# Kernel tuning notes

Measured on AMD Instinct MI355X. Metric: run time of the kernel, lower is better.

The kernel has to match this reference:

```python
import jax, jax.numpy as jnp
import numpy as np

B, LQ, LK, C = 16, 1024, 1024, 512
WH = int(LQ ** 0.5)  # 32


def setup_inputs() -> dict:
    key = jax.random.key(0)
    ks = jax.random.split(key, 6)
    s1 = 1.0 / np.sqrt(LK)
    return {
        "query": jax.random.normal(ks[0], (B, LQ, C), jnp.float32),
        "key": jax.random.normal(ks[1], (B, LK, C), jnp.float32),
        "value": jax.random.normal(ks[2], (B, LK, C), jnp.float32),
        # nn.Linear weights, stored [out_features, in_features] like torch
        "w1": jax.random.normal(ks[3], (LK, LK), jnp.float32) * s1,
        "w2": jax.random.normal(ks[4], (LK, LK), jnp.float32) * s1,
        "w3": jax.random.normal(ks[5], (1, LK), jnp.float32) * s1,
    }


def reference(query, key, value, w1, w2, w3):
    # cosine-similarity matrix (computed under no_grad in the original)
    q = query / 100.0
    k = key / 100.0
    qn = jnp.sqrt(jnp.sum(q * q, axis=-1))[:, :, None]   # [B, LQ, 1]
    kn = jnp.sqrt(jnp.sum(k * k, axis=-1))[:, None, :]   # [B, 1, LK]
    outer = qn * kn                                       # rank-1 outer product [B, LQ, LK]
    upper = jnp.einsum('bqc,bkc->bqk', q, k)              # [B, LQ, LK]
    similar_rev = jax.lax.stop_gradient(upper / (outer + 1e-6))

    # 3-layer MLP gating over the LK axis -> scalar weight per query row
    h = jax.nn.gelu(jnp.einsum('bqk,ok->bqo', similar_rev, w1), approximate=False)
    h = jax.nn.gelu(jnp.einsum('bqk,ok->bqo', h, w2), approximate=False)
    w = jnp.einsum('bqk,ok->bqo', h, w3)[..., 0]          # [B, LQ]

    # weight^T @ similar_rev / wh, then tanh -> per-key scalar gate [B, LK, 1]
    weight = jnp.einsum('bq,bqk->bk', w, similar_rev) / WH
    weight = jnp.tanh(weight)[:, :, None]

    # value modulation + residual
    return value * weight + value
```

## Files before the change

kernel.cpp:

```cpp
#include <hip/hip_runtime.h>
#include <hip/hip_bf16.h>

#define B_  16
#define LQ_ 1024
#define LK_ 1024
#define C_  512

typedef __attribute__((ext_vector_type(4))) float f32x4;
typedef __attribute__((ext_vector_type(8))) short bf16x8;

__device__ __forceinline__ float bf2f(ushort u) {
  union { unsigned int i; float f; } v; v.i = ((unsigned int)u) << 16; return v.f;
}
__device__ __forceinline__ ushort f2bf(float f) {
  union { float f; unsigned int i; } v; v.f = f;
  unsigned int r = v.i + 0x7fffu + ((v.i >> 16) & 1u);
  return (ushort)(r >> 16);
}
__device__ __forceinline__ float gelu_exact(float x) {
  return 0.5f * x * (1.0f + erff(x * 0.70710678118654752f));
}

__global__ __launch_bounds__(256) void prep_qk(const float* __restrict__ x,
                                               ushort* __restrict__ xb,
                                               float* __restrict__ norms) {
  int wid = blockIdx.x * 4 + (threadIdx.x >> 6);
  int lane = threadIdx.x & 63;
  const float* xr = x + (long)wid * C_;
  ushort* xo = xb + (long)wid * C_;
  float ss = 0.f;
#pragma unroll
  for (int i0 = 0; i0 < 2; ++i0) {
    int i = lane * 4 + i0 * 256;
    float4 v = *(const float4*)(xr + i);
    ss += v.x * v.x + v.y * v.y + v.z * v.z + v.w * v.w;
    ushort4 o;
    o.x = f2bf(v.x); o.y = f2bf(v.y); o.z = f2bf(v.z); o.w = f2bf(v.w);
    *(ushort4*)(xo + i) = o;
  }
#pragma unroll
  for (int off = 32; off > 0; off >>= 1) ss += __shfl_xor(ss, off);
  if (lane == 0) norms[wid] = sqrtf(ss);
}

__global__ __launch_bounds__(256) void conv_bf16(const float* __restrict__ x,
                                                 ushort* __restrict__ o, int n4) {
  int i = blockIdx.x * 256 + threadIdx.x;
  if (i < n4) {
    float4 v = *(const float4*)(x + (long)i * 4);
    ushort4 u;
    u.x = f2bf(v.x); u.y = f2bf(v.y); u.z = f2bf(v.z); u.w = f2bf(v.w);
    *(ushort4*)(o + (long)i * 4) = u;
  }
}

#define BK 32
#define LDT 40

template <int EPI>
__global__ __launch_bounds__(256, 2) void gemm_nt(
    const ushort* __restrict__ A, const ushort* __restrict__ Bm,
    ushort* __restrict__ Cc, int K, long sA, long sB, long sC,
    const float* __restrict__ qn, const float* __restrict__ kn) {
  int b = blockIdx.z;
  A += (long)b * sA;
  Bm += (long)b * sB;
  Cc += (long)b * sC;
  const int bm = blockIdx.y * 128, bn = blockIdx.x * 128;

  __shared__ ushort At[128][LDT];
  __shared__ ushort Bt[128][LDT];

  int tid = threadIdx.x;
  int lane = tid & 63, w = tid >> 6;
  int wr = w >> 1, wc = w & 1;
  int l16 = lane & 15, lhi = lane >> 4;

  f32x4 acc[4][4] = {};

  for (int k0 = 0; k0 < K; k0 += BK) {
    __syncthreads();
#pragma unroll
    for (int i = 0; i < 2; ++i) {
      int chunk = tid + 256 * i;
      int row = chunk >> 2, cb = chunk & 3;
      *(bf16x8*)&At[row][cb * 8] =
          *(const bf16x8*)(A + (long)(bm + row) * K + k0 + cb * 8);
      *(bf16x8*)&Bt[row][cb * 8] =
          *(const bf16x8*)(Bm + (long)(bn + row) * K + k0 + cb * 8);
    }
    __syncthreads();

    bf16x8 af[4], bfr[4];
#pragma unroll
    for (int m = 0; m < 4; ++m)
      af[m] = *(const bf16x8*)&At[wr * 64 + m * 16 + l16][lhi * 8];
#pragma unroll
    for (int n = 0; n < 4; ++n)
      bfr[n] = *(const bf16x8*)&Bt[wc * 64 + n * 16 + l16][lhi * 8];
#pragma unroll
    for (int m = 0; m < 4; ++m)
#pragma unroll
      for (int n = 0; n < 4; ++n)
        acc[m][n] = __builtin_amdgcn_mfma_f32_16x16x32_bf16(af[m], bfr[n],
                                                            acc[m][n], 0, 0, 0);
  }

#pragma unroll
  for (int m = 0; m < 4; ++m) {
    int row0 = bm + wr * 64 + m * 16 + lhi * 4;
#pragma unroll
    for (int n = 0; n < 4; ++n) {
      int col = bn + wc * 64 + n * 16 + l16;
#pragma unroll
      for (int r = 0; r < 4; ++r) {
        float v = acc[m][n][r];
        int grow = row0 + r;
        if (EPI == 0) {
          v = v / (qn[grow] * kn[col] + 1e-2f);
        } else {
          v = gelu_exact(v);
        }
        Cc[(long)grow * 1024 + col] = f2bf(v);
      }
    }
  }
}

__global__ __launch_bounds__(256) void wdot(const ushort* __restrict__ h2,
                                            const float* __restrict__ w3,
                                            float* __restrict__ wv) {
  int row = blockIdx.x * 4 + (threadIdx.x >> 6);
  int lane = threadIdx.x & 63;
  const ushort* hr = h2 + (long)row * LK_;
  float acc = 0.f;
#pragma unroll
  for (int i = 0; i < 2; ++i) {
    int idx = (lane + 64 * i) * 8;
    bf16x8 v = *(const bf16x8*)(hr + idx);
#pragma unroll
    for (int j = 0; j < 8; ++j) acc += bf2f((ushort)v[j]) * w3[idx + j];
  }
#pragma unroll
  for (int off = 32; off > 0; off >>= 1) acc += __shfl_xor(acc, off);
  if (lane == 0) wv[row] = acc;
}

__global__ __launch_bounds__(256) void gate_partial(const ushort* __restrict__ S,
                                                    const float* __restrict__ wv,
                                                    float* __restrict__ wraw) {
  int b = blockIdx.z;
  int k = blockIdx.x * 256 + threadIdx.x;
  int q0 = blockIdx.y * 128;
  const ushort* Sb = S + (long)b * LQ_ * LK_;
  const float* wb = wv + b * LQ_;
  float acc = 0.f;
#pragma unroll 4
  for (int q = q0; q < q0 + 128; ++q) acc += wb[q] * bf2f(Sb[(long)q * LK_ + k]);
  atomicAdd(&wraw[b * LK_ + k], acc);
}

__global__ __launch_bounds__(256) void finalize(const float* __restrict__ value,
                                                const float* __restrict__ wraw,
                                                float* __restrict__ out) {
  long i = (long)blockIdx.x * 256 + threadIdx.x;
  long e = i * 4;
  int row = (int)(e >> 9);
  float g = 1.f + tanhf(wraw[row] * (1.f / 32.f));
  float4 v = ((const float4*)value)[i];
  v.x *= g; v.y *= g; v.z *= g; v.w *= g;
  ((float4*)out)[i] = v;
}

extern "C" void kernel_launch(void* const* d_in, const int* in_sizes, int n_in,
                              void* d_out, int out_size, void* d_ws,
                              size_t ws_size, hipStream_t stream) {
  const float* query = (const float*)d_in[0];
  const float* key   = (const float*)d_in[1];
  const float* value = (const float*)d_in[2];
  const float* w1    = (const float*)d_in[3];
  const float* w2    = (const float*)d_in[4];
  const float* w3    = (const float*)d_in[5];
  float* out = (float*)d_out;

  const size_t QB_BYTES = (size_t)B_ * LQ_ * C_ * 2;
  const size_t S_BYTES  = (size_t)B_ * LQ_ * LK_ * 2;
  const size_t W_BYTES  = (size_t)LK_ * LK_ * 2;
  const size_t OFF_QB = 0;
  const size_t OFF_KB = OFF_QB + QB_BYTES;
  const size_t OFF_H2 = 0;
  const size_t OFF_S  = OFF_KB + QB_BYTES;
  const size_t OFF_H1 = OFF_S + S_BYTES;
  const size_t OFF_W1 = OFF_H1 + S_BYTES;
  const size_t OFF_W2 = OFF_W1 + W_BYTES;
  const size_t OFF_QN = OFF_W2 + W_BYTES;
  const size_t OFF_KN = OFF_QN + (size_t)B_ * LQ_ * 4;
  const size_t OFF_WV = OFF_KN + (size_t)B_ * LK_ * 4;
  const size_t OFF_WR = OFF_WV + (size_t)B_ * LQ_ * 4;
  const size_t TOTAL  = OFF_WR + (size_t)B_ * LK_ * 4;
  if (ws_size < TOTAL) return;

  char* ws = (char*)d_ws;
  ushort* Qb  = (ushort*)(ws + OFF_QB);
  ushort* Kb  = (ushort*)(ws + OFF_KB);
  ushort* S   = (ushort*)(ws + OFF_S);
  ushort* h1  = (ushort*)(ws + OFF_H1);
  ushort* h2  = (ushort*)(ws + OFF_H2);
  ushort* W1b = (ushort*)(ws + OFF_W1);
  ushort* W2b = (ushort*)(ws + OFF_W2);
  float* qn   = (float*)(ws + OFF_QN);
  float* kn   = (float*)(ws + OFF_KN);
  float* wv   = (float*)(ws + OFF_WV);
  float* wraw = (float*)(ws + OFF_WR);

  prep_qk<<<dim3(B_ * LQ_ / 4), 256, 0, stream>>>(query, Qb, qn);
  prep_qk<<<dim3(B_ * LK_ / 4), 256, 0, stream>>>(key, Kb, kn);
  conv_bf16<<<dim3(LK_ * LK_ / 4 / 256), 256, 0, stream>>>(w1, W1b, LK_ * LK_ / 4);
  conv_bf16<<<dim3(LK_ * LK_ / 4 / 256), 256, 0, stream>>>(w2, W2b, LK_ * LK_ / 4);
  hipMemsetAsync(wraw, 0, (size_t)B_ * LK_ * 4, stream);

  gemm_nt<0><<<dim3(8, 8, B_), 256, 0, stream>>>(
      Qb, Kb, S, C_, (long)LQ_ * C_, (long)LK_ * C_, (long)LQ_ * LK_, qn, kn);

  gemm_nt<1><<<dim3(8, 8, B_), 256, 0, stream>>>(
      S, W1b, h1, LK_, (long)LQ_ * LK_, 0L, (long)LQ_ * LK_, nullptr, nullptr);

  gemm_nt<1><<<dim3(8, 8, B_), 256, 0, stream>>>(
      h1, W2b, h2, LK_, (long)LQ_ * LK_, 0L, (long)LQ_ * LK_, nullptr, nullptr);

  wdot<<<dim3(B_ * LQ_ / 4), 256, 0, stream>>>(h2, w3, wv);

  gate_partial<<<dim3(LK_ / 256, LQ_ / 128, B_), 256, 0, stream>>>(S, wv, wraw);

  finalize<<<dim3((size_t)B_ * LK_ * C_ / 4 / 256), 256, 0, stream>>>(value, wraw, out);
}
```

Baseline: 202.9 us.

## Rewrite GEMMs as 256x256 double-buffered direct-to-LDS tiles and fuse w3 dot

Replaces the 128x128 single-buffered GEMM with a 256x256 tile, 512-thread kernel. It uses global_load_lds direct-to-LDS loads, XOR-swizzled LDS, double buffering with prefetch interleaved with MFMA phases, and s_setprio. It remaps the grid so blocks of the same batch land on the same XCD for L2 reuse. The third GEMM's epilogue now applies GELU and the w3 dot product with atomics into wv, which removes the h2 write and the separate wdot kernel. The risks are 256 blocks giving only one wave of occupancy on 256 CUs, atomic summation order, and LDS usage of 128KB per block.

```diff
diff --git a/kernel.cpp b/kernel.cpp
--- a/kernel.cpp
+++ b/kernel.cpp
@@ -19,6 +19,12 @@
 }
 __device__ __forceinline__ float gelu_exact(float x) {
   return 0.5f * x * (1.0f + erff(x * 0.70710678118654752f));
+}
+
+__device__ __forceinline__ void gload_lds16(const ushort* g, ushort* l) {
+  __builtin_amdgcn_global_load_lds(
+      (const __attribute__((address_space(1))) void*)g,
+      (__attribute__((address_space(3))) void*)l, 16, 0, 0);
 }
 
 __global__ __launch_bounds__(256) void prep_qk(const float* __restrict__ x,
@@ -54,96 +60,164 @@
   }
 }
 
-#define BK 32
-#define LDT 40
-
 template <int EPI>
-__global__ __launch_bounds__(256, 2) void gemm_nt(
+__global__ __launch_bounds__(512, 2) void gemm256(
     const ushort* __restrict__ A, const ushort* __restrict__ Bm,
     ushort* __restrict__ Cc, int K, long sA, long sB, long sC,
-    const float* __restrict__ qn, const float* __restrict__ kn) {
-  int b = blockIdx.z;
+    const float* __restrict__ qn, const float* __restrict__ kn,
+    const float* __restrict__ w3v, float* __restrict__ wv) {
+  int per = (int)(gridDim.x >> 3);
+  int orig = blockIdx.x;
+  int id = (orig & 7) * per + (orig >> 3);
+  int b = id >> 4;
+  int rt = id & 15;
+  const int bm = (rt >> 2) * 256, bn = (rt & 3) * 256;
+
   A += (long)b * sA;
   Bm += (long)b * sB;
-  Cc += (long)b * sC;
-  const int bm = blockIdx.y * 128, bn = blockIdx.x * 128;
-
-  __shared__ ushort At[128][LDT];
-  __shared__ ushort Bt[128][LDT];
-
-  int tid = threadIdx.x;
-  int lane = tid & 63, w = tid >> 6;
-  int wr = w >> 1, wc = w & 1;
-  int l16 = lane & 15, lhi = lane >> 4;
-
-  f32x4 acc[4][4] = {};
-
-  for (int k0 = 0; k0 < K; k0 += BK) {
-    __syncthreads();
-#pragma unroll
-    for (int i = 0; i < 2; ++i) {
-      int chunk = tid + 256 * i;
-      int row = chunk >> 2, cb = chunk & 3;
-      *(bf16x8*)&At[row][cb * 8] =
-          *(const bf16x8*)(A + (long)(bm + row) * K + k0 + cb * 8);
-      *(bf16x8*)&Bt[row][cb * 8] =
-          *(const bf16x8*)(Bm + (long)(bn + row) * K + k0 + cb * 8);
+
+  __shared__ ushort At[2][256][64];
+  __shared__ ushort Bt[2][256][64];
+  const int bufStride = 256 * 64;
+
+  const int tid = threadIdx.x;
+  const int lane = tid & 63, w = tid >> 6;
+  const int wr = w >> 2, wc = w & 3;
+  const int l16 = lane & 15, lhi = lane >> 4;
+
+  f32x4 acc[8][4] = {};
+
+  const ushort* gA[4];
+  const ushort* gB[4];
+  ushort* lA[4];
+  ushort* lB[4];
+#pragma unroll
+  for (int i = 0; i < 4; ++i) {
+    int c = i * 512 + tid;
+    int row = c >> 3;
+    int cb = (c & 7) ^ (row & 7);
+    gA[i] = A + (long)(bm + row) * K + cb * 8;
+    gB[i] = Bm + (long)(bn + row) * K + cb * 8;
+    int wch = i * 512 + (tid & ~63);
+    lA[i] = &At[0][0][0] + (size_t)wch * 8;
+    lB[i] = &Bt[0][0][0] + (size_t)wch * 8;
+  }
+
+#pragma unroll
+  for (int i = 0; i < 4; ++i) {
+    gload_lds16(gA[i], lA[i]);
+    gload_lds16(gB[i], lB[i]);
+  }
+  asm volatile("s_waitcnt vmcnt(0)" ::: "memory");
+  __builtin_amdgcn_s_barrier();
+
+  const int nt = K / 64;
+  int cur = 0;
+  for (int t = 0; t < nt; ++t) {
+    const int koff = (t + 1) * 64;
+    const bool pf = (t + 1 < nt);
+    const ushort* Acur = &At[cur][0][0];
+    const ushort* Bcur = &Bt[cur][0][0];
+    const size_t nxo = (size_t)(cur ^ 1) * bufStride;
+
+    bf16x8 bfr[4][2];
+
+#pragma unroll
+    for (int p = 0; p < 4; ++p) {
+      bf16x8 af[2][2];
+#pragma unroll
+      for (int e = 0; e < 2; ++e)
+#pragma unroll
+        for (int kk = 0; kk < 2; ++kk) {
+          int r = wr * 128 + (p * 2 + e) * 16 + l16;
+          af[e][kk] = *(const bf16x8*)(Acur + r * 64 +
+                                       (((kk * 4 + lhi) ^ (r & 7)) * 8));
+        }
+      if (p == 0) {
+#pragma unroll
+        for (int n = 0; n < 4; ++n)
+#pragma unroll
+          for (int kk = 0; kk < 2; ++kk) {
+            int r = wc * 64 + n * 16 + l16;
+            bfr[n][kk] = *(const bf16x8*)(Bcur + r * 64 +
+                                          (((kk * 4 + lhi) ^ (r & 7)) * 8));
+          }
+      }
+      if (pf) {
+        if (p == 0) {
+          gload_lds16(gA[0] + koff, lA[0] + nxo);
+          gload_lds16(gA[1] + koff, lA[1] + nxo);
+          gload_lds16(gB[0] + koff, lB[0] + nxo);
+        } else if (p == 1) {
+          gload_lds16(gA[2] + koff, lA[2] + nxo);
+          gload_lds16(gA[3] + koff, lA[3] + nxo);
+          gload_lds16(gB[1] + koff, lB[1] + nxo);
+        } else if (p == 2) {
+          gload_lds16(gB[2] + koff, lB[2] + nxo);
+          gload_lds16(gB[3] + koff, lB[3] + nxo);
+        }
+      }
+      __builtin_amdgcn_s_barrier();
+      __builtin_amdgcn_s_setprio(1);
+#pragma unroll
+      for (int e = 0; e < 2; ++e)
+#pragma unroll
+        for (int n = 0; n < 4; ++n)
+#pragma unroll
+          for (int kk = 0; kk < 2; ++kk)
+            acc[p * 2 + e][n] = __builtin_amdgcn_mfma_f32_16x16x32_bf16(
+                af[e][kk], bfr[n][kk], acc[p * 2 + e][n], 0, 0, 0);
+      __builtin_amdgcn_s_setprio(0);
+      if (p == 3) asm volatile("s_waitcnt vmcnt(0)" ::: "memory");
+      __builtin_amdgcn_s_barrier();
     }
-    __syncthreads();
-
-    bf16x8 af[4], bfr[4];
-#pragma unroll
-    for (int m = 0; m < 4; ++m)
-      af[m] = *(const bf16x8*)&At[wr * 64 + m * 16 + l16][lhi * 8];
-#pragma unroll
-    for (int n = 0; n < 4; ++n)
-      bfr[n] = *(const bf16x8*)&Bt[wc * 64 + n * 16 + l16][lhi * 8];
-#pragma unroll
-    for (int m = 0; m < 4; ++m)
-#pragma unroll
-      for (int n = 0; n < 4; ++n)
-        acc[m][n] = __builtin_amdgcn_mfma_f32_16x16x32_bf16(af[m], bfr[n],
-                                                            acc[m][n], 0, 0, 0);
-  }
-
-#pragma unroll
-  for (int m = 0; m < 4; ++m) {
-    int row0 = bm + wr * 64 + m * 16 + lhi * 4;
-#pragma unroll
-    for (int n = 0; n < 4; ++n) {
-      int col = bn + wc * 64 + n * 16 + l16;
-#pragma unroll
-      for (int r = 0; r < 4; ++r) {
-        float v = acc[m][n][r];
-        int grow = row0 + r;
-        if (EPI == 0) {
-          v = v / (qn[grow] * kn[col] + 1e-2f);
-        } else {
-          v = gelu_exact(v);
+    cur ^= 1;
+  }
+
+  if constexpr (EPI == 2) {
+    float* wvb = wv + (long)b * LQ_;
+    float w3c[4];
+#pragma unroll
+    for (int n = 0; n < 4; ++n) w3c[n] = w3v[bn + wc * 64 + n * 16 + l16];
+#pragma unroll
+    for (int m = 0; m < 8; ++m)
+#pragma unroll
+      for (int rr = 0; rr < 4; ++rr) {
+        float s = 0.f;
+#pragma unroll
+        for (int n = 0; n < 4; ++n)
+          s += gelu_exact(acc[m][n][rr]) * w3c[n];
+        s += __shfl_xor(s, 1);
+        s += __shfl_xor(s, 2);
+        s += __shfl_xor(s, 4);
+        s += __shfl_xor(s, 8);
+        if (l16 == 0)
+          atomicAdd(&wvb[bm + wr * 128 + m * 16 + lhi * 4 + rr], s);
+      }
+  } else {
+    Cc += (long)b * sC;
+    const float* qnb = qn + (long)b * LQ_;
+    const float* knb = kn + (long)b * LK_;
+#pragma unroll
+    for (int m = 0; m < 8; ++m) {
+      int row0 = bm + wr * 128 + m * 16 + lhi * 4;
+#pragma unroll
+      for (int n = 0; n < 4; ++n) {
+        int col = bn + wc * 64 + n * 16 + l16;
+#pragma unroll
+        for (int rr = 0; rr < 4; ++rr) {
+          float v = acc[m][n][rr];
+          int grow = row0 + rr;
+          if (EPI == 0) {
+            v = v / (qnb[grow] * knb[col] + 1e-2f);
+          } else {
+            v = gelu_exact(v);
+          }
+          Cc[(long)grow * 1024 + col] = f2bf(v);
         }
-        Cc[(long)grow * 1024 + col] = f2bf(v);
       }
     }
   }
-}
-
-__global__ __launch_bounds__(256) void wdot(const ushort* __restrict__ h2,
-                                            const float* __restrict__ w3,
-                                            float* __restrict__ wv) {
-  int row = blockIdx.x * 4 + (threadIdx.x >> 6);
-  int lane = threadIdx.x & 63;
-  const ushort* hr = h2 + (long)row * LK_;
-  float acc = 0.f;
-#pragma unroll
-  for (int i = 0; i < 2; ++i) {
-    int idx = (lane + 64 * i) * 8;
-    bf16x8 v = *(const bf16x8*)(hr + idx);
-#pragma unroll
-    for (int j = 0; j < 8; ++j) acc += bf2f((ushort)v[j]) * w3[idx + j];
-  }
-#pragma unroll
-  for (int off = 32; off > 0; off >>= 1) acc += __shfl_xor(acc, off);
-  if (lane == 0) wv[row] = acc;
 }
 
 __global__ __launch_bounds__(256) void gate_partial(const ushort* __restrict__ S,
@@ -188,7 +262,6 @@
   const size_t W_BYTES  = (size_t)LK_ * LK_ * 2;
   const size_t OFF_QB = 0;
   const size_t OFF_KB = OFF_QB + QB_BYTES;
-  const size_t OFF_H2 = 0;
   const size_t OFF_S  = OFF_KB + QB_BYTES;
   const size_t OFF_H1 = OFF_S + S_BYTES;
   const size_t OFF_W1 = OFF_H1 + S_BYTES;
@@ -205,7 +278,6 @@
   ushort* Kb  = (ushort*)(ws + OFF_KB);
   ushort* S   = (ushort*)(ws + OFF_S);
   ushort* h1  = (ushort*)(ws + OFF_H1);
-  ushort* h2  = (ushort*)(ws + OFF_H2);
   ushort* W1b = (ushort*)(ws + OFF_W1);
   ushort* W2b = (ushort*)(ws + OFF_W2);
   float* qn   = (float*)(ws + OFF_QN);
@@ -218,17 +290,19 @@
   conv_bf16<<<dim3(LK_ * LK_ / 4 / 256), 256, 0, stream>>>(w1, W1b, LK_ * LK_ / 4);
   conv_bf16<<<dim3(LK_ * LK_ / 4 / 256), 256, 0, stream>>>(w2, W2b, LK_ * LK_ / 4);
   hipMemsetAsync(wraw, 0, (size_t)B_ * LK_ * 4, stream);
-
-  gemm_nt<0><<<dim3(8, 8, B_), 256, 0, stream>>>(
-      Qb, Kb, S, C_, (long)LQ_ * C_, (long)LK_ * C_, (long)LQ_ * LK_, qn, kn);
-
-  gemm_nt<1><<<dim3(8, 8, B_), 256, 0, stream>>>(
-      S, W1b, h1, LK_, (long)LQ_ * LK_, 0L, (long)LQ_ * LK_, nullptr, nullptr);
-
-  gemm_nt<1><<<dim3(8, 8, B_), 256, 0, stream>>>(
-      h1, W2b, h2, LK_, (long)LQ_ * LK_, 0L, (long)LQ_ * LK_, nullptr, nullptr);
-
-  wdot<<<dim3(B_ * LQ_ / 4), 256, 0, stream>>>(h2, w3, wv);
+  hipMemsetAsync(wv, 0, (size_t)B_ * LQ_ * 4, stream);
+
+  gemm256<0><<<dim3(256), 512, 0, stream>>>(
+      Qb, Kb, S, C_, (long)LQ_ * C_, (long)LK_ * C_, (long)LQ_ * LK_,
+      qn, kn, nullptr, nullptr);
+
+  gemm256<1><<<dim3(256), 512, 0, stream>>>(
+      S, W1b, h1, LK_, (long)LQ_ * LK_, 0L, (long)LQ_ * LK_,
+      nullptr, nullptr, nullptr, nullptr);
+
+  gemm256<2><<<dim3(256), 512, 0, stream>>>(
+      h1, W2b, nullptr, LK_, (long)LQ_ * LK_, 0L, 0L,
+      nullptr, nullptr, w3, wv);
 
   gate_partial<<<dim3(LK_ / 256, LQ_ / 128, B_), 256, 0, stream>>>(S, wv, wraw);
 
```

Measured after the change: 170.2 us. -16.1%, faster.
